# Optimization experiments

Measured on AMD Instinct MI355X. Metric: run time of the kernel, lower is better.

Reference implementation:

```python
import jax, jax.numpy as jnp
import numpy as np

N, T, D, H = 2, 2048, 1024, 16
DH = D // H  # per-head dim = 64


def setup_inputs() -> dict:
    key = jax.random.key(0)
    k1, k2, k3, k4 = jax.random.split(key, 4)
    x = jax.random.normal(k1, (N, T, D), dtype=jnp.float32)
    W = jax.random.normal(k2, (D, 3 * D), dtype=jnp.float32) * (D ** -0.5)
    proj_w = jax.random.normal(k3, (D, D), dtype=jnp.float32) * (D ** -0.5)
    proj_b = jax.random.normal(k4, (D,), dtype=jnp.float32) * 0.02
    return {"x": x, "W": W, "proj_w": proj_w, "proj_b": proj_b}


def reference(x, W, proj_w, proj_b):
    n, t, d = x.shape
    qkv = x @ W                                   # [N,T,3D]
    q, k, v = jnp.split(qkv, 3, axis=-1)          # each [N,T,D]
    def heads(a):
        return a.reshape(n, t, H, DH).transpose(0, 2, 1, 3)  # [N,H,T,DH]
    q, k, v = heads(q), heads(k), heads(v)
    scale = DH ** -0.5
    scores = jnp.einsum('nhtd,nhsd->nhts', q, k) * scale      # [N,H,T,T]
    causal = jnp.tril(jnp.ones((t, t), dtype=bool))
    scores = jnp.where(causal, scores, jnp.finfo(scores.dtype).min)
    w = jax.nn.softmax(scores, axis=-1)
    out = jnp.einsum('nhts,nhsd->nhtd', w, v)                 # [N,H,T,DH]
    out = out.transpose(0, 2, 1, 3).reshape(n, t, d)          # [N,T,D]
    return out @ proj_w.T + proj_b
```

## Files before the change

kernel.cpp:

```cpp
#include <hip/hip_runtime.h>
#include <hip/hip_bf16.h>
#include <stdint.h>

#define N_B 2
#define T_S 2048
#define D_M 1024
#define H_N 16
#define D_H 64

typedef __bf16 bf16_t;
typedef __bf16 bf16x8 __attribute__((ext_vector_type(8)));
typedef float f32x4 __attribute__((ext_vector_type(4)));
typedef float f32x16 __attribute__((ext_vector_type(16)));

__device__ __forceinline__ void async_ld16(const void* g, void* lds_uniform_base) {
  __builtin_amdgcn_global_load_lds(
      (const __attribute__((address_space(1))) uint32_t*)(uintptr_t)g,
      (__attribute__((address_space(3))) uint32_t*)(uintptr_t)lds_uniform_base,
      16, 0, 0);
}

__global__ __launch_bounds__(256) void prep_kernel(
    const float* __restrict__ x, bf16_t* __restrict__ x_bf,
    const float* __restrict__ pw, bf16_t* __restrict__ pwb,
    const float* __restrict__ W, bf16_t* __restrict__ Wt) {
  __shared__ float tile[32][33];
  const int bid = blockIdx.x;
  if (bid < 5120) {
    int i = bid * 256 + threadIdx.x;
    const float* in = x;
    bf16_t* out = x_bf;
    const int n1 = (4096 * 1024) / 4;
    if (i >= n1) { i -= n1; in = pw; out = pwb; }
    float4 v = ((const float4*)in)[i];
    union { bf16_t b[4]; uint64_t u; } o;
    o.b[0] = (bf16_t)v.x; o.b[1] = (bf16_t)v.y;
    o.b[2] = (bf16_t)v.z; o.b[3] = (bf16_t)v.w;
    *(uint64_t*)(out + (size_t)i * 4) = o.u;
  } else {
    const int tb = bid - 5120;
    const int bx = (tb % 96) * 32;
    const int by = (tb / 96) * 32;
    const int tx = threadIdx.x & 31, ty = threadIdx.x >> 5;
#pragma unroll
    for (int i = 0; i < 32; i += 8)
      tile[ty + i][tx] = W[(size_t)(by + ty + i) * 3072 + bx + tx];
    __syncthreads();
#pragma unroll
    for (int i = 0; i < 32; i += 8)
      Wt[(size_t)(bx + ty + i) * 1024 + by + tx] = (bf16_t)tile[tx][ty + i];
  }
}

template <int MODE>
__global__ __launch_bounds__(256) void gemm_bt_kernel(
    const bf16_t* __restrict__ A, const bf16_t* __restrict__ Bt,
    bf16_t* __restrict__ Qo, bf16_t* __restrict__ Ko, bf16_t* __restrict__ Vto,
    const float* __restrict__ bias, float* __restrict__ Co,
    int nbx, int cpx) {
  __shared__ bf16_t As[2][4096];
  __shared__ bf16_t Bs[2][4096];
  const int tid = threadIdx.x;
  const int lane = tid & 63;
  const int wid = tid >> 6;
  const int wr = wid >> 1, wc = wid & 1;
  const int g = lane >> 4, lr = lane & 15;
  const int d_ = blockIdx.x;
  const int orig = (d_ & 7) * cpx + (d_ >> 3);
  const int brow = (orig / nbx) * 128;
  const int bcol = (orig % nbx) * 128;

  f32x4 acc[4][4] = {};

  const int idx0 = wid * 128 + lane;
  const int idx1 = wid * 128 + 64 + lane;
  const int row0 = idx0 >> 2, part0 = (idx0 & 3) * 8;
  const int row1 = idx1 >> 2, part1 = (idx1 & 3) * 8;
  const int dst0 = (wid * 128) * 8;
  const int dst1 = (wid * 128 + 64) * 8;

  auto stage = [&](int t, int b) {
    async_ld16(A + (size_t)(brow + row0) * 1024 + t * 32 + part0, &As[b][dst0]);
    async_ld16(Bt + (size_t)(bcol + row0) * 1024 + t * 32 + part0, &Bs[b][dst0]);
    async_ld16(A + (size_t)(brow + row1) * 1024 + t * 32 + part1, &As[b][dst1]);
    async_ld16(Bt + (size_t)(bcol + row1) * 1024 + t * 32 + part1, &Bs[b][dst1]);
  };

  stage(0, 0);
  for (int t = 0; t < 32; ++t) {
    if (t + 1 < 32) {
      stage(t + 1, (t + 1) & 1);
      asm volatile("s_waitcnt vmcnt(4)" ::: "memory");
    } else {
      asm volatile("s_waitcnt vmcnt(0)" ::: "memory");
    }
    __builtin_amdgcn_s_barrier();
    __builtin_amdgcn_sched_barrier(0);

    const bf16_t* as = As[t & 1];
    const bf16_t* bs = Bs[t & 1];
    bf16x8 af[4], bfr[4];
#pragma unroll
    for (int i = 0; i < 4; ++i) {
      af[i]  = *(const bf16x8*)&as[(wr * 64 + i * 16 + lr) * 32 + g * 8];
      bfr[i] = *(const bf16x8*)&bs[(wc * 64 + i * 16 + lr) * 32 + g * 8];
    }
    __builtin_amdgcn_s_setprio(1);
#pragma unroll
    for (int i = 0; i < 4; ++i)
#pragma unroll
      for (int j = 0; j < 4; ++j)
        acc[i][j] = __builtin_amdgcn_mfma_f32_16x16x32_bf16(af[i], bfr[j], acc[i][j], 0, 0, 0);
    __builtin_amdgcn_s_setprio(0);
    asm volatile("s_waitcnt lgkmcnt(0)" ::: "memory");
    __builtin_amdgcn_s_barrier();
  }

#pragma unroll
  for (int i = 0; i < 4; ++i) {
    int row0_ = brow + wr * 64 + i * 16 + g * 4;
#pragma unroll
    for (int j = 0; j < 4; ++j) {
      int col = bcol + wc * 64 + j * 16 + lr;
#pragma unroll
      for (int r = 0; r < 4; ++r) {
        int row = row0_ + r;
        float v = acc[i][j][r];
        if (MODE == 0) {
          int n = row >> 11, t = row & (T_S - 1);
          int which = col >> 10, d = col & (D_M - 1);
          int h = d >> 6, dh = d & 63;
          if (which == 0)
            Qo[((size_t)(n * H_N + h) * T_S + t) * D_H + dh] = (bf16_t)v;
          else if (which == 1)
            Ko[((size_t)(n * H_N + h) * T_S + t) * D_H + dh] = (bf16_t)v;
          else
            Vto[((size_t)(n * H_N + h) * D_H + dh) * T_S + t] = (bf16_t)v;
        } else {
          Co[(size_t)row * D_M + col] = v + bias[col];
        }
      }
    }
  }
}

__global__ __launch_bounds__(256, 4) void attn_kernel(const bf16_t* __restrict__ Q,
                                                      const bf16_t* __restrict__ K,
                                                      const bf16_t* __restrict__ Vt,
                                                      bf16_t* __restrict__ O) {
  __shared__ bf16_t Ks[2][4096];
  __shared__ bf16_t Vs[2][4096];
  __shared__ float Linv[64];

  const int tid = threadIdx.x;
  const int lane = tid & 63;
  const int w = tid >> 6;
  const int qsub = w >> 1, khalf = w & 1;
  const int l31 = lane & 31;
  const int hi = lane >> 5;

  const int d_ = blockIdx.x;
  const int x = d_ & 7;
  const int s = d_ >> 3;
  const int hs = s & 3, j_ = s >> 2;
  const int t_ = j_ >> 3, m_ = j_ & 7;
  const int qc = (t_ == 0) ? (31 - m_) : (t_ == 1) ? (16 + m_)
               : (t_ == 2) ? (15 - m_) : m_;
  const int nh = x * 4 + hs;
  const bf16_t* Qg = Q + (size_t)nh * T_S * D_H;
  const char* Kb = (const char*)(K + (size_t)nh * T_S * D_H);
  const char* Vb = (const char*)(Vt + (size_t)nh * D_H * T_S);
  const int n = nh >> 4, h = nh & 15;

  const int c0 = (w * 2 + 0) * 64 + lane;
  const int c1 = (w * 2 + 1) * 64 + lane;
  const int r0_ = c0 >> 3, cb0 = (c0 & 7) * 16, sw0 = (r0_ & 7) << 4;
  const int r1_ = c1 >> 3, cb1 = (c1 & 7) * 16, sw1 = (r1_ & 7) << 4;
  const int koff0 = r0_ * 128 + (cb0 ^ sw0), koff1 = r1_ * 128 + (cb1 ^ sw1);
  const int voff0 = r0_ * 4096 + (cb0 ^ sw0), voff1 = r1_ * 4096 + (cb1 ^ sw1);
  const int lds0 = (w * 2 + 0) * 1024, lds1 = (w * 2 + 1) * 1024;

  const int q0w = qc * 64 + qsub * 32;
  const int nt = qc + 1;

  bf16x8 qf[4];
#pragma unroll
  for (int ksd = 0; ksd < 4; ++ksd) {
    bf16x8 t = *(const bf16x8*)(Qg + (size_t)(q0w + l31) * D_H + ksd * 16 + hi * 8);
#pragma unroll
    for (int e = 0; e < 8; ++e) t[e] = (bf16_t)((float)t[e] * 0.125f);
    qf[ksd] = t;
  }

  const int kabs_ = khalf * 32 + l31;
  int kfo[4];
#pragma unroll
  for (int ksd = 0; ksd < 4; ++ksd)
    kfo[ksd] = (kabs_ * 128 + ksd * 32 + hi * 16) ^ ((kabs_ & 7) << 4);
  int vfo[2][2];
#pragma unroll
  for (int db = 0; db < 2; ++db)
#pragma unroll
    for (int kk = 0; kk < 2; ++kk) {
      int dd = db * 32 + l31;
      vfo[db][kk] = (dd * 128 + khalf * 64 + kk * 32 + hi * 16) ^ ((dd & 7) << 4);
    }

  f32x16 oacc[2] = {};
  float lsum = 0.f;

  auto issue = [&](int t, int b) {
    const char* kt_ = Kb + (size_t)t * 8192;
    const char* vt_ = Vb + (size_t)t * 128;
    async_ld16(kt_ + koff0, (char*)Ks[b] + lds0);
    async_ld16(kt_ + koff1, (char*)Ks[b] + lds1);
    async_ld16(vt_ + voff0, (char*)Vs[b] + lds0);
    async_ld16(vt_ + voff1, (char*)Vs[b] + lds1);
  };

  auto compute = [&](int kt, int b, bool domask) {
    f32x16 S = {};
    __builtin_amdgcn_s_setprio(1);
#pragma unroll
    for (int ksd = 0; ksd < 4; ++ksd) {
      bf16x8 kf = *(const bf16x8*)((char*)Ks[b] + kfo[ksd]);
      S = __builtin_amdgcn_mfma_f32_32x32x16_bf16(kf, qf[ksd], S, 0, 0, 0);
    }
    __builtin_amdgcn_s_setprio(0);

    if (domask) {
#pragma unroll
      for (int r = 0; r < 16; ++r) {
        int ktile = khalf * 32 + (r & 3) + 8 * (r >> 2) + 4 * hi;
        if (kt * 64 + ktile > q0w + l31) S[r] = -1.0e30f;
      }
    }

    float p[16];
#pragma unroll
    for (int r = 0; r < 16; ++r) {
      p[r] = __builtin_amdgcn_exp2f(fminf(S[r] * 1.442695041f, 50.f));
      lsum += p[r];
    }

    uint32_t dw[8];
#pragma unroll
    for (int i = 0; i < 8; ++i) {
      union { bf16_t b2[2]; uint32_t u; } pk;
      pk.b2[0] = (bf16_t)p[2 * i];
      pk.b2[1] = (bf16_t)p[2 * i + 1];
      dw[i] = pk.u;
    }

    bf16x8 pa[2];
#pragma unroll
    for (int kk = 0; kk < 2; ++kk) {
      uint32_t u0 = dw[kk * 4 + 0], u1 = dw[kk * 4 + 1];
      uint32_t u2 = dw[kk * 4 + 2], u3 = dw[kk * 4 + 3];
      uint32_t sa = __shfl_xor(hi ? u0 : u2, 32, 64);
      uint32_t sb = __shfl_xor(hi ? u1 : u3, 32, 64);
      union { uint32_t u[4]; bf16x8 v; } f;
      f.u[0] = hi ? sa : u0;
      f.u[1] = hi ? sb : u1;
      f.u[2] = hi ? u2 : sa;
      f.u[3] = hi ? u3 : sb;
      pa[kk] = f.v;
    }

    __builtin_amdgcn_s_setprio(1);
#pragma unroll
    for (int db = 0; db < 2; ++db)
#pragma unroll
      for (int kk = 0; kk < 2; ++kk) {
        bf16x8 vf = *(const bf16x8*)((char*)Vs[b] + vfo[db][kk]);
        oacc[db] = __builtin_amdgcn_mfma_f32_32x32x16_bf16(pa[kk], vf, oacc[db], 0, 0, 0);
      }
    __builtin_amdgcn_s_setprio(0);
  };

  issue(0, 0);
  int buf = 0;
  for (int kt = 0; kt < nt; ++kt) {
    asm volatile("s_waitcnt vmcnt(0)" ::: "memory");
    __builtin_amdgcn_s_barrier();
    __builtin_amdgcn_sched_barrier(0);
    if (kt + 1 < nt) issue(kt + 1, buf ^ 1);
    compute(kt, buf, kt == nt - 1);
    buf ^= 1;
  }

  lsum += __shfl_xor(lsum, 32, 64);

  __syncthreads();
  float* mO = (float*)Ks;
  float* mL = (float*)Vs;
  if (khalf == 1) {
    float* ob = mO + qsub * 2048;
#pragma unroll
    for (int db = 0; db < 2; ++db)
#pragma unroll
      for (int r = 0; r < 16; ++r)
        ob[(db * 16 + r) * 64 + lane] = oacc[db][r];
    mL[qsub * 32 + l31] = lsum;
  }
  __syncthreads();
  if (khalf == 0) {
    float* ob = mO + qsub * 2048;
    float ltot = lsum + mL[qsub * 32 + l31];
    Linv[qsub * 32 + l31] = 1.f / ltot;
#pragma unroll
    for (int db = 0; db < 2; ++db)
#pragma unroll
      for (int r = 0; r < 16; ++r)
        oacc[db][r] += ob[(db * 16 + r) * 64 + lane];
#pragma unroll
    for (int r = 0; r < 16; ++r) {
      int ro = (r & 3) + 8 * (r >> 2) + 4 * hi;
      int qrow = q0w + ro;
      float inv = Linv[qsub * 32 + ro];
#pragma unroll
      for (int db = 0; db < 2; ++db)
        O[(size_t)(n * T_S + qrow) * D_M + h * D_H + db * 32 + l31] =
            (bf16_t)(oacc[db][r] * inv);
    }
  }
}

extern "C" void kernel_launch(void* const* d_in, const int* in_sizes, int n_in,
                              void* d_out, int out_size, void* d_ws, size_t ws_size,
                              hipStream_t stream) {
  const float* x  = (const float*)d_in[0];
  const float* W  = (const float*)d_in[1];
  const float* pw = (const float*)d_in[2];
  const float* pb = (const float*)d_in[3];
  float* out = (float*)d_out;

  char* ws = (char*)d_ws;
  bf16_t* x_bf = (bf16_t*)(ws);
  bf16_t* Wt   = (bf16_t*)(ws + (8ull  << 20));
  bf16_t* pwb  = (bf16_t*)(ws + (14ull << 20));
  bf16_t* Qh   = (bf16_t*)(ws + (16ull << 20));
  bf16_t* Kh   = (bf16_t*)(ws + (24ull << 20));
  bf16_t* Vth  = (bf16_t*)(ws + (32ull << 20));
  bf16_t* Oa   = (bf16_t*)(ws + (40ull << 20));

  prep_kernel<<<8192, 256, 0, stream>>>(x, x_bf, pw, pwb, W, Wt);

  gemm_bt_kernel<0><<<768, 256, 0, stream>>>(x_bf, Wt, Qh, Kh, Vth, nullptr, nullptr, 24, 96);

  attn_kernel<<<1024, 256, 0, stream>>>(Qh, Kh, Vth, Oa);

  gemm_bt_kernel<1><<<256, 256, 0, stream>>>(Oa, pwb, nullptr, nullptr, nullptr, pb, out, 8, 32);
}
```

Baseline: 102.3 us.

## Template GEMM tile height, use 64-row tiles for output projection, remap XCD blocks

Makes the GEMM tile height a template parameter. The output projection now uses 64x128 tiles with 512 blocks instead of 256, so more of the GPU's compute units are filled. The QKV GEMM gets a new block-to-XCD mapping that gives each XCD a contiguous 2D region of tiles for better L2 reuse. The load staging is generalized to a per-thread list of chunk addresses. The smaller tiles lower arithmetic intensity per block in exchange for occupancy.

```diff
diff --git a/kernel.cpp b/kernel.cpp
--- a/kernel.cpp
+++ b/kernel.cpp
@@ -52,62 +52,81 @@
   }
 }
 
-template <int MODE>
+template <int MODE, int BM>
 __global__ __launch_bounds__(256) void gemm_bt_kernel(
     const bf16_t* __restrict__ A, const bf16_t* __restrict__ Bt,
     bf16_t* __restrict__ Qo, bf16_t* __restrict__ Ko, bf16_t* __restrict__ Vto,
-    const float* __restrict__ bias, float* __restrict__ Co,
-    int nbx, int cpx) {
-  __shared__ bf16_t As[2][4096];
-  __shared__ bf16_t Bs[2][4096];
+    const float* __restrict__ bias, float* __restrict__ Co) {
+  constexpr int MI = BM / 32;
+  constexpr int ABYTES = BM * 64;
+  constexpr int NLD = BM / 64 + 2;
+  __shared__ char lds[2][ABYTES + 8192];
+
   const int tid = threadIdx.x;
   const int lane = tid & 63;
   const int wid = tid >> 6;
   const int wr = wid >> 1, wc = wid & 1;
   const int g = lane >> 4, lr = lane & 15;
   const int d_ = blockIdx.x;
-  const int orig = (d_ & 7) * cpx + (d_ >> 3);
-  const int brow = (orig / nbx) * 128;
-  const int bcol = (orig % nbx) * 128;
-
-  f32x4 acc[4][4] = {};
-
-  const int idx0 = wid * 128 + lane;
-  const int idx1 = wid * 128 + 64 + lane;
-  const int row0 = idx0 >> 2, part0 = (idx0 & 3) * 8;
-  const int row1 = idx1 >> 2, part1 = (idx1 & 3) * 8;
-  const int dst0 = (wid * 128) * 8;
-  const int dst1 = (wid * 128 + 64) * 8;
+
+  int brow, bcol;
+  if (MODE == 0) {
+    const int xcd = d_ & 7, i_ = d_ >> 3;
+    const int rx = xcd >> 1, cx = xcd & 1;
+    brow = ((rx << 3) + i_ / 12) * 128;
+    bcol = (cx * 12 + i_ % 12) * 128;
+  } else {
+    const int orig = (d_ & 7) * 64 + (d_ >> 3);
+    brow = (orig >> 3) * 64;
+    bcol = (orig & 7) * 128;
+  }
+
+  f32x4 acc[MI][4] = {};
+
+  const char* gbase[NLD];
+  int sdst[NLD];
+#pragma unroll
+  for (int q = 0; q < NLD; ++q) {
+    int c = q * 256 + tid;
+    if (c < BM * 4) {
+      gbase[q] = (const char*)A + (size_t)(brow + (c >> 2)) * 2048 + (c & 3) * 16;
+      sdst[q] = c * 16;
+    } else {
+      int cb = c - BM * 4;
+      gbase[q] = (const char*)Bt + (size_t)(bcol + (cb >> 2)) * 2048 + (cb & 3) * 16;
+      sdst[q] = ABYTES + cb * 16;
+    }
+  }
 
   auto stage = [&](int t, int b) {
-    async_ld16(A + (size_t)(brow + row0) * 1024 + t * 32 + part0, &As[b][dst0]);
-    async_ld16(Bt + (size_t)(bcol + row0) * 1024 + t * 32 + part0, &Bs[b][dst0]);
-    async_ld16(A + (size_t)(brow + row1) * 1024 + t * 32 + part1, &As[b][dst1]);
-    async_ld16(Bt + (size_t)(bcol + row1) * 1024 + t * 32 + part1, &Bs[b][dst1]);
+#pragma unroll
+    for (int q = 0; q < NLD; ++q)
+      async_ld16(gbase[q] + t * 64, lds[b] + sdst[q]);
   };
 
   stage(0, 0);
   for (int t = 0; t < 32; ++t) {
     if (t + 1 < 32) {
       stage(t + 1, (t + 1) & 1);
-      asm volatile("s_waitcnt vmcnt(4)" ::: "memory");
+      if constexpr (NLD == 4) { asm volatile("s_waitcnt vmcnt(4)" ::: "memory"); }
+      else                    { asm volatile("s_waitcnt vmcnt(3)" ::: "memory"); }
     } else {
       asm volatile("s_waitcnt vmcnt(0)" ::: "memory");
     }
     __builtin_amdgcn_s_barrier();
     __builtin_amdgcn_sched_barrier(0);
 
-    const bf16_t* as = As[t & 1];
-    const bf16_t* bs = Bs[t & 1];
-    bf16x8 af[4], bfr[4];
-#pragma unroll
-    for (int i = 0; i < 4; ++i) {
-      af[i]  = *(const bf16x8*)&as[(wr * 64 + i * 16 + lr) * 32 + g * 8];
-      bfr[i] = *(const bf16x8*)&bs[(wc * 64 + i * 16 + lr) * 32 + g * 8];
-    }
+    const char* base = lds[t & 1];
+    bf16x8 af[MI], bfr[4];
+#pragma unroll
+    for (int i = 0; i < MI; ++i)
+      af[i] = *(const bf16x8*)(base + (wr * (BM / 2) + i * 16 + lr) * 64 + g * 16);
+#pragma unroll
+    for (int j = 0; j < 4; ++j)
+      bfr[j] = *(const bf16x8*)(base + ABYTES + (wc * 64 + j * 16 + lr) * 64 + g * 16);
     __builtin_amdgcn_s_setprio(1);
 #pragma unroll
-    for (int i = 0; i < 4; ++i)
+    for (int i = 0; i < MI; ++i)
 #pragma unroll
       for (int j = 0; j < 4; ++j)
         acc[i][j] = __builtin_amdgcn_mfma_f32_16x16x32_bf16(af[i], bfr[j], acc[i][j], 0, 0, 0);
@@ -117,8 +136,8 @@
   }
 
 #pragma unroll
-  for (int i = 0; i < 4; ++i) {
-    int row0_ = brow + wr * 64 + i * 16 + g * 4;
+  for (int i = 0; i < MI; ++i) {
+    int row0_ = brow + wr * (BM / 2) + i * 16 + g * 4;
 #pragma unroll
     for (int j = 0; j < 4; ++j) {
       int col = bcol + wc * 64 + j * 16 + lr;
@@ -346,9 +365,9 @@
 
   prep_kernel<<<8192, 256, 0, stream>>>(x, x_bf, pw, pwb, W, Wt);
 
-  gemm_bt_kernel<0><<<768, 256, 0, stream>>>(x_bf, Wt, Qh, Kh, Vth, nullptr, nullptr, 24, 96);
+  gemm_bt_kernel<0, 128><<<768, 256, 0, stream>>>(x_bf, Wt, Qh, Kh, Vth, nullptr, nullptr);
 
   attn_kernel<<<1024, 256, 0, stream>>>(Qh, Kh, Vth, Oa);
 
-  gemm_bt_kernel<1><<<256, 256, 0, stream>>>(Oa, pwb, nullptr, nullptr, nullptr, pb, out, 8, 32);
-}
+  gemm_bt_kernel<1, 64><<<512, 256, 0, stream>>>(Oa, pwb, nullptr, nullptr, nullptr, pb, out);
+}
```

Measured after the change: 108.6 us. 6.2% more time.
